# Optimization experiments

Hardware: AMD Instinct MI355X
Metric: run time of the kernel (lower is better)

## Reference

```python
import jax, jax.numpy as jnp
from jax import lax
import numpy as np

IN, H1, H2 = 16, 64, 1


def _init_lstm(key, in_dim, hid):
    k = 1.0 / np.sqrt(hid)
    k1, k2, k3, k4 = jax.random.split(key, 4)
    u = lambda kk, shp: jax.random.uniform(kk, shp, jnp.float32, -k, k)
    return u(k1, (4 * hid, in_dim)), u(k2, (4 * hid, hid)), u(k3, (4 * hid,)), u(k4, (4 * hid,))


def setup_inputs() -> dict:
    key = jax.random.key(0)
    kx, k1, k2, kf = jax.random.split(key, 4)
    x = jax.random.normal(kx, (4096, 256, IN), jnp.float32)
    w_ih1, w_hh1, b_ih1, b_hh1 = _init_lstm(k1, IN, H1)
    w_ih2, w_hh2, b_ih2, b_hh2 = _init_lstm(k2, H1, H2)
    kfw, kfb = jax.random.split(kf)
    fc_w = jax.random.uniform(kfw, (1, 1), jnp.float32, -1.0, 1.0)
    fc_b = jax.random.uniform(kfb, (1,), jnp.float32, -1.0, 1.0)
    return {"x": x,
            "w_ih1": w_ih1, "w_hh1": w_hh1, "b_ih1": b_ih1, "b_hh1": b_hh1,
            "w_ih2": w_ih2, "w_hh2": w_hh2, "b_ih2": b_ih2, "b_hh2": b_hh2,
            "fc_w": fc_w, "fc_b": fc_b}


def _lstm(x, w_ih, w_hh, b_ih, b_hh):
    # x: [B, T, in]; PyTorch gate order: i, f, g, o
    B = x.shape[0]
    H = w_hh.shape[1]
    # precompute input projection for all timesteps (big GEMM outside recurrence)
    xg = jnp.einsum('bti,gi->btg', x, w_ih) + b_ih + b_hh  # [B, T, 4H]

    def step(carry, xg_t):
        h, c = carry
        gates = xg_t + h @ w_hh.T  # [B, 4H]
        i, f, g, o = jnp.split(gates, 4, axis=-1)
        i = jax.nn.sigmoid(i)
        f = jax.nn.sigmoid(f)
        g = jnp.tanh(g)
        o = jax.nn.sigmoid(o)
        c = f * c + i * g
        h = o * jnp.tanh(c)
        return (h, c), h

    h0 = jnp.zeros((B, H), x.dtype)
    (_, _), hs = lax.scan(step, (h0, h0), jnp.swapaxes(xg, 0, 1))  # hs: [T, B, H]
    return jnp.swapaxes(hs, 0, 1)  # [B, T, H]


def reference(x, w_ih1, w_hh1, b_ih1, b_hh1, w_ih2, w_hh2, b_ih2, b_hh2, fc_w, fc_b):
    h = _lstm(x, w_ih1, w_hh1, b_ih1, b_hh1)   # [B, T, 64]
    h = _lstm(h, w_ih2, w_hh2, b_ih2, b_hh2)   # [B, T, 1]
    return h @ fc_w.T + fc_b                     # [B, T, 1]
```

## Files before the change

### kernel.cpp

```cpp
#include <hip/hip_runtime.h>

typedef float  f32x4  __attribute__((ext_vector_type(4)));
typedef __bf16 bf16x8 __attribute__((ext_vector_type(8)));
typedef unsigned short u16x8 __attribute__((ext_vector_type(8)));

#define NL2E (-1.44269504088896f)
#define TL2E ( 2.88539008177793f)

__device__ __forceinline__ float rcpf(float x) { return __builtin_amdgcn_rcpf(x); }
__device__ __forceinline__ float ex2(float x)  { return __builtin_amdgcn_exp2f(x); }

__device__ __forceinline__ float cell_update(float zi, float zf, float zg, float zo, float& c) {
    const float Ei = ex2(zi), Ef = ex2(zf), Eg = ex2(zg), Eo = ex2(zo);
    const float ig = (Eg - 1.0f) * rcpf((1.0f + Ei) * (1.0f + Eg));
    const float fv = rcpf(1.0f + Ef);
    c = __builtin_fmaf(fv, c, ig);
    const float zc = fminf(fmaxf(TL2E * c, -60.0f), 60.0f);
    const float Ec = ex2(zc);
    return (Ec - 1.0f) * rcpf((1.0f + Eo) * (1.0f + Ec));
}

__global__ __launch_bounds__(256, 1) void lstm_fused(
    const float* __restrict__ x,
    const float* __restrict__ w_ih1,
    const float* __restrict__ w_hh1,
    const float* __restrict__ b_ih1, const float* __restrict__ b_hh1,
    const float* __restrict__ w_ih2,
    const float* __restrict__ w_hh2,
    const float* __restrict__ b_ih2, const float* __restrict__ b_hh2,
    const float* __restrict__ fc_w, const float* __restrict__ fc_b,
    float* __restrict__ out)
{
    __shared__ unsigned short A_h[2 * 16 * 64];
    __shared__ unsigned short Xc[2 * 16 * 16 * 32];
    __shared__ float Pre2[2][64];
    __shared__ float Ybuf[16][16];

    const int tid = threadIdx.x;
    const int wv  = tid >> 6;
    const int l   = tid & 63;
    const int q   = l & 15;
    const int hi  = l >> 4;
    const int b0  = blockIdx.x << 4;
    const int he  = (wv << 4) + q;
    const int sw  = (q & 7) << 4;

    ((u16x8*)A_h)[tid] = (u16x8){0,0,0,0,0,0,0,0};

    bf16x8 Bf[4][3];
    #pragma unroll
    for (int g = 0; g < 4; ++g) {
        const float sc = (g == 2) ? TL2E : NL2E;
        const int n = (g << 6) + (wv << 4) + q;
        #pragma unroll
        for (int ks = 0; ks < 3; ++ks) {
            bf16x8 tmp;
            #pragma unroll
            for (int j = 0; j < 8; ++j) {
                const int k = ks * 32 + hi * 8 + j;
                float v = 0.f;
                if (k < 64)      v = w_hh1[n * 64 + k];
                else if (k < 80) v = w_ih1[n * 16 + (k - 64)];
                tmp[j] = (__bf16)(sc * v);
            }
            Bf[g][ks] = tmp;
        }
    }
    bf16x8 B2[2];
    {
        const float sc2 = (q == 2) ? TL2E : NL2E;
        #pragma unroll
        for (int ks = 0; ks < 2; ++ks) {
            bf16x8 tmp;
            #pragma unroll
            for (int j = 0; j < 8; ++j) {
                const int k = ks * 32 + hi * 8 + j;
                const float v = (q < 4) ? w_ih2[q * 64 + k] : 0.f;
                tmp[j] = (__bf16)(sc2 * v);
            }
            B2[ks] = tmp;
        }
    }

    float accb[4];
    #pragma unroll
    for (int g = 0; g < 4; ++g) {
        const float sc = (g == 2) ? TL2E : NL2E;
        accb[g] = sc * (b_ih1[(g << 6) + he] + b_hh1[(g << 6) + he]);
    }

    const float w2si = NL2E * w_hh2[0], w2sf = NL2E * w_hh2[1];
    const float w2sg = TL2E * w_hh2[2], w2so = NL2E * w_hh2[3];
    const float nb2i = NL2E * (b_ih2[0] + b_hh2[0]);
    const float nb2f = NL2E * (b_ih2[1] + b_hh2[1]);
    const float tb2g = TL2E * (b_ih2[2] + b_hh2[2]);
    const float nb2o = NL2E * (b_ih2[3] + b_hh2[3]);
    const float fcw = fc_w[0], fcb = fc_b[0];

    const int bx = tid >> 4, part = tid & 15;
    const int swx = (bx & 7) << 4;
    const unsigned xo0 = (unsigned)(bx * 1024 + (((part << 6) +  0) ^ swx));
    const unsigned xo1 = (unsigned)(bx * 1024 + (((part << 6) + 16) ^ swx));
    const unsigned xo2 = (unsigned)(bx * 1024 + (((part << 6) + 32) ^ swx));
    const unsigned xo3 = (unsigned)(bx * 1024 + (((part << 6) + 48) ^ swx));
    const float* xrow = x + (size_t)(b0 + bx) * 4096 + part * 16;

    f32x4 xq0, xq1, xq2, xq3;
    auto stage_x = [&](int bufoff) {
        bf16x8 lo, hw;
        #pragma unroll
        for (int j = 0; j < 4; ++j) {
            lo[j] = (__bf16)xq0[j]; lo[4 + j] = (__bf16)xq1[j];
            hw[j] = (__bf16)xq2[j]; hw[4 + j] = (__bf16)xq3[j];
        }
        const u16x8 z = {0,0,0,0,0,0,0,0};
        char* base = (char*)Xc + bufoff;
        *(u16x8*)(base + xo0) = __builtin_bit_cast(u16x8, lo);
        *(u16x8*)(base + xo1) = __builtin_bit_cast(u16x8, hw);
        *(u16x8*)(base + xo2) = z;
        *(u16x8*)(base + xo3) = z;
    };

    xq0 = ((const f32x4*)xrow)[0]; xq1 = ((const f32x4*)xrow)[1];
    xq2 = ((const f32x4*)xrow)[2]; xq3 = ((const f32x4*)xrow)[3];
    stage_x(0);
    {
        const float* p = xrow + 256;
        xq0 = ((const f32x4*)p)[0]; xq1 = ((const f32x4*)p)[1];
        xq2 = ((const f32x4*)p)[2]; xq3 = ((const f32x4*)p)[3];
    }

    const unsigned ar0 = (unsigned)((q * 128 +      hi * 16) ^ sw);
    const unsigned ar1 = (unsigned)((q * 128 + 64 + hi * 16) ^ sw);
    unsigned awb[4];
    #pragma unroll
    for (int j = 0; j < 4; ++j) {
        const int b = (hi << 2) + j;
        awb[j] = (unsigned)(b * 128 + ((he * 2) ^ ((b & 7) << 4)));
    }

    float c1[4] = {0.f, 0.f, 0.f, 0.f};
    float h2 = 0.f, c2 = 0.f;

    __syncthreads();

    u16x8 ra2cur = *(const u16x8*)((const char*)Xc + ((q * 1024 + (hi << 4)) ^ sw));

    #pragma unroll 2
    for (int t = 0; t < 256; ++t) {
        const int tt = t & 15;
        if (tt == 0 && t + 16 < 256) {
            stage_x(((((t >> 4) + 1) & 1)) << 14);
            if (t + 32 < 256) {
                const float* p = xrow + (t + 32) * 16;
                xq0 = ((const f32x4*)p)[0]; xq1 = ((const f32x4*)p)[1];
                xq2 = ((const f32x4*)p)[2]; xq3 = ((const f32x4*)p)[3];
            }
        }

        const int rb = ((t + 1) & 1) << 11;
        const u16x8 ra0 = *(const u16x8*)((const char*)A_h + rb + ar0);
        const u16x8 ra1 = *(const u16x8*)((const char*)A_h + rb + ar1);
        const int tn = (t < 255) ? t + 1 : t;
        const u16x8 ra2nxt = *(const u16x8*)((const char*)Xc + (((tn >> 4) & 1) << 14)
                               + ((q * 1024 + ((tn & 15) << 6) + (hi << 4)) ^ sw));
        f32x4 p2;
        if (wv == 1) p2 = *(const f32x4*)&Pre2[(t + 1) & 1][(l & 15) << 2];

        const bf16x8 a2 = __builtin_bit_cast(bf16x8, ra2cur);
        f32x4 g0 = {accb[0], accb[0], accb[0], accb[0]};
        f32x4 g1 = {accb[1], accb[1], accb[1], accb[1]};
        f32x4 g2 = {accb[2], accb[2], accb[2], accb[2]};
        f32x4 g3 = {accb[3], accb[3], accb[3], accb[3]};
        g0 = __builtin_amdgcn_mfma_f32_16x16x32_bf16(a2, Bf[0][2], g0, 0, 0, 0);
        g1 = __builtin_amdgcn_mfma_f32_16x16x32_bf16(a2, Bf[1][2], g1, 0, 0, 0);
        g2 = __builtin_amdgcn_mfma_f32_16x16x32_bf16(a2, Bf[2][2], g2, 0, 0, 0);
        g3 = __builtin_amdgcn_mfma_f32_16x16x32_bf16(a2, Bf[3][2], g3, 0, 0, 0);
        const bf16x8 a0 = __builtin_bit_cast(bf16x8, ra0);
        g0 = __builtin_amdgcn_mfma_f32_16x16x32_bf16(a0, Bf[0][0], g0, 0, 0, 0);
        g1 = __builtin_amdgcn_mfma_f32_16x16x32_bf16(a0, Bf[1][0], g1, 0, 0, 0);
        g2 = __builtin_amdgcn_mfma_f32_16x16x32_bf16(a0, Bf[2][0], g2, 0, 0, 0);
        g3 = __builtin_amdgcn_mfma_f32_16x16x32_bf16(a0, Bf[3][0], g3, 0, 0, 0);
        const bf16x8 a1 = __builtin_bit_cast(bf16x8, ra1);
        g0 = __builtin_amdgcn_mfma_f32_16x16x32_bf16(a1, Bf[0][1], g0, 0, 0, 0);
        g1 = __builtin_amdgcn_mfma_f32_16x16x32_bf16(a1, Bf[1][1], g1, 0, 0, 0);
        g2 = __builtin_amdgcn_mfma_f32_16x16x32_bf16(a1, Bf[2][1], g2, 0, 0, 0);
        g3 = __builtin_amdgcn_mfma_f32_16x16x32_bf16(a1, Bf[3][1], g3, 0, 0, 0);

        if (wv == 3) {
            f32x4 p4 = {0.f, 0.f, 0.f, 0.f};
            p4 = __builtin_amdgcn_mfma_f32_16x16x32_bf16(a0, B2[0], p4, 0, 0, 0);
            p4 = __builtin_amdgcn_mfma_f32_16x16x32_bf16(a1, B2[1], p4, 0, 0, 0);
            if (q < 4) {
                #pragma unroll
                for (int r = 0; r < 4; ++r) Pre2[t & 1][((hi << 2) + r) * 4 + q] = p4[r];
            }
        }

        if (wv == 1 && t >= 2) {
            const int s = t - 2;
            if (l < 16) {
                const float zi = p2[0] + __builtin_fmaf(w2si, h2, nb2i);
                const float zf = p2[1] + __builtin_fmaf(w2sf, h2, nb2f);
                const float zg = p2[2] + __builtin_fmaf(w2sg, h2, tb2g);
                const float zo = p2[3] + __builtin_fmaf(w2so, h2, nb2o);
                h2 = cell_update(zi, zf, zg, zo, c2);
                Ybuf[l][s & 15] = __builtin_fmaf(fcw, h2, fcb);
            }
            if ((s & 15) == 15) {
                float* op = out + (size_t)(b0 + (l >> 2)) * 256 + (s - 15) + ((l & 3) << 2);
                *(f32x4*)op = *(const f32x4*)&Ybuf[l >> 2][(l & 3) << 2];
            }
        }

        float Ei[4], Ef[4], Eg[4], Eo[4];
        #pragma unroll
        for (int j = 0; j < 4; ++j) Ei[j] = ex2(g0[j]);
        #pragma unroll
        for (int j = 0; j < 4; ++j) Ef[j] = ex2(g1[j]);
        #pragma unroll
        for (int j = 0; j < 4; ++j) Eg[j] = ex2(g2[j]);
        #pragma unroll
        for (int j = 0; j < 4; ++j) Eo[j] = ex2(g3[j]);
        char* AW = (char*)A_h + ((t & 1) << 11);
        #pragma unroll
        for (int j = 0; j < 4; ++j) {
            const float ig = (Eg[j] - 1.0f) * rcpf((1.0f + Ei[j]) * (1.0f + Eg[j]));
            const float fv = rcpf(1.0f + Ef[j]);
            c1[j] = __builtin_fmaf(fv, c1[j], ig);
            const float zc = fminf(fmaxf(TL2E * c1[j], -60.0f), 60.0f);
            const float Ec = ex2(zc);
            const float hv = (Ec - 1.0f) * rcpf((1.0f + Eo[j]) * (1.0f + Ec));
            *(unsigned short*)(AW + awb[j]) = __builtin_bit_cast(unsigned short, (__bf16)hv);
        }

        ra2cur = ra2nxt;
        __syncthreads();
    }

    if (wv == 3) {
        const u16x8 ra0 = *(const u16x8*)((const char*)A_h + 2048 + ar0);
        const u16x8 ra1 = *(const u16x8*)((const char*)A_h + 2048 + ar1);
        f32x4 p4 = {0.f, 0.f, 0.f, 0.f};
        p4 = __builtin_amdgcn_mfma_f32_16x16x32_bf16(__builtin_bit_cast(bf16x8, ra0), B2[0], p4, 0, 0, 0);
        p4 = __builtin_amdgcn_mfma_f32_16x16x32_bf16(__builtin_bit_cast(bf16x8, ra1), B2[1], p4, 0, 0, 0);
        if (q < 4) {
            #pragma unroll
            for (int r = 0; r < 4; ++r) Pre2[0][((hi << 2) + r) * 4 + q] = p4[r];
        }
    }
    __syncthreads();
    if (wv == 1) {
        if (l < 16) {
            #pragma unroll
            for (int e = 0; e < 2; ++e) {
                const f32x4 p2 = *(const f32x4*)&Pre2[1 - e][l << 2];
                const float zi = p2[0] + __builtin_fmaf(w2si, h2, nb2i);
                const float zf = p2[1] + __builtin_fmaf(w2sf, h2, nb2f);
                const float zg = p2[2] + __builtin_fmaf(w2sg, h2, tb2g);
                const float zo = p2[3] + __builtin_fmaf(w2so, h2, nb2o);
                h2 = cell_update(zi, zf, zg, zo, c2);
                Ybuf[l][14 + e] = __builtin_fmaf(fcw, h2, fcb);
            }
        }
        float* op = out + (size_t)(b0 + (l >> 2)) * 256 + 240 + ((l & 3) << 2);
        *(f32x4*)op = *(const f32x4*)&Ybuf[l >> 2][(l & 3) << 2];
    }
}

extern "C" void kernel_launch(void* const* d_in, const int* in_sizes, int n_in,
                              void* d_out, int out_size, void* d_ws, size_t ws_size,
                              hipStream_t stream) {
    (void)in_sizes; (void)n_in; (void)out_size; (void)d_ws; (void)ws_size;
    const float* x     = (const float*)d_in[0];
    const float* w_ih1 = (const float*)d_in[1];
    const float* w_hh1 = (const float*)d_in[2];
    const float* b_ih1 = (const float*)d_in[3];
    const float* b_hh1 = (const float*)d_in[4];
    const float* w_ih2 = (const float*)d_in[5];
    const float* w_hh2 = (const float*)d_in[6];
    const float* b_ih2 = (const float*)d_in[7];
    const float* b_hh2 = (const float*)d_in[8];
    const float* fc_w  = (const float*)d_in[9];
    const float* fc_b  = (const float*)d_in[10];
    lstm_fused<<<dim3(256), dim3(256), 0, stream>>>(
        x, w_ih1, w_hh1, b_ih1, b_hh1, w_ih2, w_hh2, b_ih2, b_hh2, fc_w, fc_b,
        (float*)d_out);
}
```

Baseline: 164.7 us.

## Fold LSTM bias into MFMA via constant-one input column, trim loop overhead

Layer-1 bias moves into the weight fragment at k=80, and a constant 1.0 bf16 is written once into the padded x staging buffer, so the MFMA chain starts from zero accumulators. The per-chunk zero-padding stores in stage_x go away because the pad region is initialized once up front. The gate activation uses the shared cell_update helper, and __syncthreads becomes a raw waitcnt plus s_barrier. The bias now passes through bf16 rounding, which costs some precision, and the hand-written barrier relies on no pending vector-memory dependencies across it.

Result: no change. 167.2 us (+1.5%).

```diff
diff --git a/kernel.cpp b/kernel.cpp
--- a/kernel.cpp
+++ b/kernel.cpp
@@ -44,8 +44,21 @@
     const int b0  = blockIdx.x << 4;
     const int he  = (wv << 4) + q;
     const int sw  = (q & 7) << 4;
-
-    ((u16x8*)A_h)[tid] = (u16x8){0,0,0,0,0,0,0,0};
+    const u16x8 z8 = {0,0,0,0,0,0,0,0};
+
+    ((u16x8*)A_h)[tid] = z8;
+    {
+        const u16x8 pad1 = {0x3F80, 0, 0, 0, 0, 0, 0, 0};
+        #pragma unroll
+        for (int r = 0; r < 2; ++r) {
+            const int idx = (tid << 1) + r;
+            const int buf = idx >> 8, pb = (idx >> 4) & 15, ptt = idx & 15;
+            char* base = (char*)Xc + (buf << 14) + pb * 1024;
+            const int swp = (pb & 7) << 4;
+            *(u16x8*)(base + ((ptt * 64 + 32) ^ swp)) = pad1;
+            *(u16x8*)(base + ((ptt * 64 + 48) ^ swp)) = z8;
+        }
+    }
 
     bf16x8 Bf[4][3];
     #pragma unroll
@@ -59,8 +72,9 @@
             for (int j = 0; j < 8; ++j) {
                 const int k = ks * 32 + hi * 8 + j;
                 float v = 0.f;
-                if (k < 64)      v = w_hh1[n * 64 + k];
-                else if (k < 80) v = w_ih1[n * 16 + (k - 64)];
+                if (k < 64)       v = w_hh1[n * 64 + k];
+                else if (k < 80)  v = w_ih1[n * 16 + (k - 64)];
+                else if (k == 80) v = b_ih1[n] + b_hh1[n];
                 tmp[j] = (__bf16)(sc * v);
             }
             Bf[g][ks] = tmp;
@@ -80,13 +94,6 @@
             }
             B2[ks] = tmp;
         }
-    }
-
-    float accb[4];
-    #pragma unroll
-    for (int g = 0; g < 4; ++g) {
-        const float sc = (g == 2) ? TL2E : NL2E;
-        accb[g] = sc * (b_ih1[(g << 6) + he] + b_hh1[(g << 6) + he]);
     }
 
     const float w2si = NL2E * w_hh2[0], w2sf = NL2E * w_hh2[1];
@@ -101,8 +108,6 @@
     const int swx = (bx & 7) << 4;
     const unsigned xo0 = (unsigned)(bx * 1024 + (((part << 6) +  0) ^ swx));
     const unsigned xo1 = (unsigned)(bx * 1024 + (((part << 6) + 16) ^ swx));
-    const unsigned xo2 = (unsigned)(bx * 1024 + (((part << 6) + 32) ^ swx));
-    const unsigned xo3 = (unsigned)(bx * 1024 + (((part << 6) + 48) ^ swx));
     const float* xrow = x + (size_t)(b0 + bx) * 4096 + part * 16;
 
     f32x4 xq0, xq1, xq2, xq3;
@@ -113,12 +118,9 @@
             lo[j] = (__bf16)xq0[j]; lo[4 + j] = (__bf16)xq1[j];
             hw[j] = (__bf16)xq2[j]; hw[4 + j] = (__bf16)xq3[j];
         }
-        const u16x8 z = {0,0,0,0,0,0,0,0};
         char* base = (char*)Xc + bufoff;
         *(u16x8*)(base + xo0) = __builtin_bit_cast(u16x8, lo);
         *(u16x8*)(base + xo1) = __builtin_bit_cast(u16x8, hw);
-        *(u16x8*)(base + xo2) = z;
-        *(u16x8*)(base + xo3) = z;
     };
 
     xq0 = ((const f32x4*)xrow)[0]; xq1 = ((const f32x4*)xrow)[1];
@@ -141,6 +143,7 @@
 
     float c1[4] = {0.f, 0.f, 0.f, 0.f};
     float h2 = 0.f, c2 = 0.f;
+    const f32x4 kz = {0.f, 0.f, 0.f, 0.f};
 
     __syncthreads();
 
@@ -168,10 +171,7 @@
         if (wv == 1) p2 = *(const f32x4*)&Pre2[(t + 1) & 1][(l & 15) << 2];
 
         const bf16x8 a2 = __builtin_bit_cast(bf16x8, ra2cur);
-        f32x4 g0 = {accb[0], accb[0], accb[0], accb[0]};
-        f32x4 g1 = {accb[1], accb[1], accb[1], accb[1]};
-        f32x4 g2 = {accb[2], accb[2], accb[2], accb[2]};
-        f32x4 g3 = {accb[3], accb[3], accb[3], accb[3]};
+        f32x4 g0 = kz, g1 = kz, g2 = kz, g3 = kz;
         g0 = __builtin_amdgcn_mfma_f32_16x16x32_bf16(a2, Bf[0][2], g0, 0, 0, 0);
         g1 = __builtin_amdgcn_mfma_f32_16x16x32_bf16(a2, Bf[1][2], g1, 0, 0, 0);
         g2 = __builtin_amdgcn_mfma_f32_16x16x32_bf16(a2, Bf[2][2], g2, 0, 0, 0);
@@ -188,7 +188,7 @@
         g3 = __builtin_amdgcn_mfma_f32_16x16x32_bf16(a1, Bf[3][1], g3, 0, 0, 0);
 
         if (wv == 3) {
-            f32x4 p4 = {0.f, 0.f, 0.f, 0.f};
+            f32x4 p4 = kz;
             p4 = __builtin_amdgcn_mfma_f32_16x16x32_bf16(a0, B2[0], p4, 0, 0, 0);
             p4 = __builtin_amdgcn_mfma_f32_16x16x32_bf16(a1, B2[1], p4, 0, 0, 0);
             if (q < 4) {
@@ -213,29 +213,15 @@
             }
         }
 
-        float Ei[4], Ef[4], Eg[4], Eo[4];
-        #pragma unroll
-        for (int j = 0; j < 4; ++j) Ei[j] = ex2(g0[j]);
-        #pragma unroll
-        for (int j = 0; j < 4; ++j) Ef[j] = ex2(g1[j]);
-        #pragma unroll
-        for (int j = 0; j < 4; ++j) Eg[j] = ex2(g2[j]);
-        #pragma unroll
-        for (int j = 0; j < 4; ++j) Eo[j] = ex2(g3[j]);
         char* AW = (char*)A_h + ((t & 1) << 11);
         #pragma unroll
         for (int j = 0; j < 4; ++j) {
-            const float ig = (Eg[j] - 1.0f) * rcpf((1.0f + Ei[j]) * (1.0f + Eg[j]));
-            const float fv = rcpf(1.0f + Ef[j]);
-            c1[j] = __builtin_fmaf(fv, c1[j], ig);
-            const float zc = fminf(fmaxf(TL2E * c1[j], -60.0f), 60.0f);
-            const float Ec = ex2(zc);
-            const float hv = (Ec - 1.0f) * rcpf((1.0f + Eo[j]) * (1.0f + Ec));
+            const float hv = cell_update(g0[j], g1[j], g2[j], g3[j], c1[j]);
             *(unsigned short*)(AW + awb[j]) = __builtin_bit_cast(unsigned short, (__bf16)hv);
         }
 
         ra2cur = ra2nxt;
-        __syncthreads();
+        asm volatile("s_waitcnt lgkmcnt(0)\n\ts_barrier" ::: "memory");
     }
 
     if (wv == 3) {
```
